# Kernel optimization log

Hardware: AMD Instinct MI355X
Metric: run time of the kernel (lower is better)

The kernel has to match this reference:

```python
import jax, jax.numpy as jnp
import numpy as np

B = 8
H_IN, W_IN = 448, 448
STRIDE = 32
NUM_CLASSES = 20
CONF_THRESH = 0.01
NMS_THRESH = 0.5
HS, WS = H_IN // STRIDE, W_IN // STRIDE  # 14, 14
N_CELLS = HS * WS  # 196
CHANNELS = [3, 64, 128, 256, 512, 512]
HEAD_OUT = 1 + NUM_CLASSES + 4  # 25


def _conv(x, w, stride):
    return jax.lax.conv_general_dilated(
        x, w, (stride, stride), 'SAME',
        dimension_numbers=('NCHW', 'OIHW', 'NCHW'))


def _create_grid():
    gy, gx = jnp.meshgrid(jnp.arange(HS), jnp.arange(WS), indexing='ij')
    return jnp.stack([gx, gy], -1).reshape(1, N_CELLS, 2).astype(jnp.float32)


def _iou_matrix(boxes):
    # boxes: [N,4] xyxy -> [N,N] pairwise IoU
    x1, y1, x2, y2 = boxes[:, 0], boxes[:, 1], boxes[:, 2], boxes[:, 3]
    area = jnp.maximum(x2 - x1, 0.0) * jnp.maximum(y2 - y1, 0.0)
    ix1 = jnp.maximum(x1[:, None], x1[None, :])
    iy1 = jnp.maximum(y1[:, None], y1[None, :])
    ix2 = jnp.minimum(x2[:, None], x2[None, :])
    iy2 = jnp.minimum(y2[:, None], y2[None, :])
    inter = jnp.maximum(ix2 - ix1, 0.0) * jnp.maximum(iy2 - iy1, 0.0)
    return inter / (area[:, None] + area[None, :] - inter + 1e-14)


def _nms_keep(scores, iou):
    # greedy per-class NMS; scores [N], iou [N,N] -> bool keep mask [N]
    order = jnp.argsort(-scores)
    iou_s = iou[order][:, order]
    idx = jnp.arange(N_CELLS)
    valid = scores[order] > CONF_THRESH

    def body(i, keep):
        sup = (iou_s[i] > NMS_THRESH) & (idx > i) & keep[i]
        return keep & (~sup)

    keep = jax.lax.fori_loop(0, N_CELLS, body, valid)
    return jnp.zeros(N_CELLS, bool).at[order].set(keep)


def setup_inputs() -> dict:
    key = jax.random.key(0)
    ks = jax.random.split(key, 8)
    x = jax.random.normal(ks[0], (B, 3, H_IN, W_IN), dtype=jnp.float32)
    params = {}
    for i in range(5):
        cin, cout = CHANNELS[i], CHANNELS[i + 1]
        std = np.sqrt(2.0 / (cin * 9))
        params[f'w{i+1}'] = jax.random.normal(ks[i + 1], (cout, cin, 3, 3), dtype=jnp.float32) * std
    std = np.sqrt(2.0 / CHANNELS[-1])
    params['w_head'] = jax.random.normal(ks[6], (HEAD_OUT, CHANNELS[-1], 1, 1), dtype=jnp.float32) * std
    return {'x': x, **params}


def reference(x, w1, w2, w3, w4, w5, w_head):
    # backbone: 5 stride-2 conv+relu stages -> stride 32
    h = x
    for w in (w1, w2, w3, w4, w5):
        h = jax.nn.relu(_conv(h, w, 2))
    pred = _conv(h, w_head, 1)                      # [B, 25, 14, 14]
    pred = pred.reshape(B, HEAD_OUT, N_CELLS).transpose(0, 2, 1)  # [B, N, 25]

    conf = jax.nn.sigmoid(pred[..., 0:1])                              # [B,N,1]
    cls_scores = jax.nn.softmax(pred[..., 1:1 + NUM_CLASSES], -1) * conf  # [B,N,C]
    txtytwth = pred[..., 1 + NUM_CLASSES:]                             # [B,N,4]

    grid = _create_grid()                                              # [1,N,2]
    xy = (jax.nn.sigmoid(txtytwth[..., :2]) + grid) * STRIDE
    wh = jnp.exp(txtytwth[..., 2:]) * STRIDE
    scale = jnp.array([W_IN, H_IN, W_IN, H_IN], dtype=jnp.float32)
    boxes = jnp.concatenate([xy - wh * 0.5, xy + wh * 0.5], -1) / scale
    boxes = jnp.clip(boxes, 0.0, 1.0)                                  # [B,N,4]

    iou = jax.vmap(_iou_matrix)(boxes)                                 # [B,N,N]
    # per-class NMS, vmapped over classes then batch
    nms_c = jax.vmap(_nms_keep, in_axes=(-1, None), out_axes=-1)       # [N,C]
    keep = jax.vmap(nms_c, in_axes=(0, 0))(cls_scores, iou)            # [B,N,C]
    final_scores = cls_scores * keep
    return jnp.concatenate([boxes, final_scores], -1)                  # [B,N,4+C]
```

## Files before the change

### kernel.cpp

```cpp
#include <hip/hip_runtime.h>
#include <math.h>

#define BATCH 8
#define NCELLS 196
#define NCLS 20
#define HEADC 25

typedef __attribute__((ext_vector_type(8))) short short8;
typedef __attribute__((ext_vector_type(4))) float f32x4;
#define MFMA16(a,b,c) __builtin_amdgcn_mfma_f32_16x16x32_bf16(a,b,c,0,0,0)

__device__ __forceinline__ unsigned short f2bf(float x) {
    union { float f; unsigned u; } a; a.f = x;
    unsigned r = a.u + 0x7FFFu + ((a.u >> 16) & 1u);
    return (unsigned short)(r >> 16);
}
__device__ __forceinline__ float bf2f(unsigned short h) {
    union { unsigned u; float f; } a; a.u = ((unsigned)h) << 16;
    return a.f;
}
__device__ __forceinline__ void split_bf(float x, unsigned short& h, unsigned short& l) {
    h = f2bf(x);
    l = f2bf(x - bf2f(h));
}

__device__ __forceinline__ void prep_one(const float* __restrict__ w, int CIN, int COUT,
                                         int idx, unsigned short* __restrict__ whi,
                                         unsigned short* __restrict__ wlo) {
    int G = COUT >> 4, CH = CIN >> 5;
    int j    = idx & 7;
    int lane = (idx >> 3) & 63;
    int fg   = idx >> 9;
    int g    = fg % G;
    int fc   = fg / G;
    int chunk = fc % CH;
    int plane = fc / CH;
    int co = g * 16 + (lane & 15);
    int ci = chunk * 32 + (lane >> 4) * 8 + j;
    int ky = plane / 3, kx = plane % 3;
    float v = w[((co * CIN + ci) * 3 + ky) * 3 + kx];
    unsigned short h, l; split_bf(v, h, l);
    whi[idx] = h; wlo[idx] = l;
}
__global__ void prep_all(const float* __restrict__ w2, const float* __restrict__ w3,
                         const float* __restrict__ w4, const float* __restrict__ w5,
                         unsigned short* __restrict__ w2h, unsigned short* __restrict__ w2l,
                         unsigned short* __restrict__ w3h, unsigned short* __restrict__ w3l,
                         unsigned short* __restrict__ w4h, unsigned short* __restrict__ w4l,
                         unsigned short* __restrict__ w5h, unsigned short* __restrict__ w5l) {
    int idx = blockIdx.x * 256 + threadIdx.x;
    const int n2 = 73728, n3 = 294912, n4 = 1179648, n5 = 2359296;
    if (idx < n2) { prep_one(w2, 64, 128, idx, w2h, w2l); return; }
    idx -= n2;
    if (idx < n3) { prep_one(w3, 128, 256, idx, w3h, w3l); return; }
    idx -= n3;
    if (idx < n4) { prep_one(w4, 256, 512, idx, w4h, w4l); return; }
    idx -= n4;
    if (idx < n5) { prep_one(w5, 512, 512, idx, w5h, w5l); }
}

__global__ void conv1_kernel(const float* __restrict__ x, const float* __restrict__ w1,
                             unsigned short* __restrict__ ohi, unsigned short* __restrict__ olo) {
    __shared__ float sW[27][64];
    __shared__ float sX[3][3][66];
    int bid = blockIdx.x;
    int xseg = bid % 7;  bid /= 7;
    int oy   = bid % 224;
    int b    = bid / 224;
    int ox0  = xseg * 32;

    for (int e = threadIdx.x; e < 1728; e += 256) {
        int k = e >> 6, co = e & 63;
        sW[k][co] = w1[co * 27 + k];
    }
    for (int e = threadIdx.x; e < 594; e += 256) {
        int ci = e / 198;
        int r  = e - ci * 198;
        int ky = r / 66;
        int lx = r - ky * 66;
        int iy = 2 * oy + ky;
        int ix = 2 * ox0 + lx;
        float v = 0.f;
        if (lx < 65 && iy < 448 && ix < 448)
            v = x[(((size_t)b * 3 + ci) * 448 + iy) * 448 + ix];
        sX[ci][ky][lx] = v;
    }
    __syncthreads();

    int pxl = threadIdx.x >> 3;
    int cog = threadIdx.x & 7;
    float acc[8] = {0.f,0.f,0.f,0.f,0.f,0.f,0.f,0.f};
    #pragma unroll
    for (int ci = 0; ci < 3; ci++) {
        #pragma unroll
        for (int ky = 0; ky < 3; ky++) {
            const float* row = sX[ci][ky];
            #pragma unroll
            for (int kx = 0; kx < 3; kx++) {
                float iv = row[2 * pxl + kx];
                int k = (ci * 3 + ky) * 3 + kx;
                float4 wa = *(const float4*)&sW[k][cog * 8];
                float4 wb = *(const float4*)&sW[k][cog * 8 + 4];
                acc[0] += wa.x * iv; acc[1] += wa.y * iv; acc[2] += wa.z * iv; acc[3] += wa.w * iv;
                acc[4] += wb.x * iv; acc[5] += wb.y * iv; acc[6] += wb.z * iv; acc[7] += wb.w * iv;
            }
        }
    }
    union { unsigned short u[8]; uint4 v; } ph, pl;
    #pragma unroll
    for (int u = 0; u < 8; u++) {
        float v = fmaxf(acc[u], 0.f);
        split_bf(v, ph.u[u], pl.u[u]);
    }
    size_t base = ((size_t)(b * 224 + oy) * 224 + ox0 + pxl) * 64 + cog * 8;
    *(uint4*)&ohi[base] = ph.v;
    *(uint4*)&olo[base] = pl.v;
}

template<int CIN, int COUT, int HIN, int WIN, int KSPLIT, bool PARTIAL>
__launch_bounds__(256, 4)
__global__ void conv_mfma(const unsigned short* __restrict__ ahi, const unsigned short* __restrict__ alo,
                          const unsigned short* __restrict__ whi, const unsigned short* __restrict__ wlo,
                          unsigned short* __restrict__ ohi, unsigned short* __restrict__ olo,
                          float* __restrict__ part) {
    constexpr int HOUT = HIN / 2, WOUT = WIN / 2;
    constexpr int TX = (WOUT + 7) / 8, TY = (HOUT + 7) / 8;
    constexpr int COG = COUT / 128;
    constexpr int CH_TOT = CIN / 32;
    constexpr int CH = CH_TOT / KSPLIT;
    constexpr int G = COUT / 16;
    constexpr int PLANE_E = 17 * 17 * 32;
    constexpr size_t PSZ = (size_t)BATCH * HOUT * WOUT * COUT;

    __shared__ __align__(16) unsigned short sA[2 * PLANE_E];

    int bid = blockIdx.x;
    int ks  = bid % KSPLIT; bid /= KSPLIT;
    int txi = bid % TX;     bid /= TX;
    int tyi = bid % TY;     bid /= TY;
    int cg  = bid % COG;
    int b   = bid / COG;
    int oy0 = tyi * 8, ox0 = txi * 8;
    int iy0 = oy0 * 2, ix0 = ox0 * 2;

    int tid = threadIdx.x;
    int w   = tid >> 6;
    int lane = tid & 63;
    int n = lane & 15, quad = lane >> 4;

    int oyl[4], oxl[4], pbase[4];
    #pragma unroll
    for (int nt = 0; nt < 4; nt++) {
        int oyq = nt >> 1, oxq = nt & 1;
        int oy_off = oyq * 4 + (n >> 2);
        int ox_off = oxq * 4 + (n & 3);
        oyl[nt] = oy0 + oy_off;
        oxl[nt] = ox0 + ox_off;
        pbase[nt] = 2 * oy_off * 17 + 2 * ox_off;
    }

    f32x4 zero = {0.f, 0.f, 0.f, 0.f};
    f32x4 acc[2][4];
    #pragma unroll
    for (int ct = 0; ct < 2; ct++)
        #pragma unroll
        for (int nt = 0; nt < 4; nt++) acc[ct][nt] = zero;

    int g0 = cg * 8 + w * 2;

    for (int ch = 0; ch < CH; ch++) {
        int chunk = ks * CH + ch;
        int ci0 = chunk * 32;
        __syncthreads();
        for (int e = tid; e < 17 * 17 * 8; e += 256) {
            int pxi = e >> 3, grp = e & 7;
            int liy = pxi / 17, lix = pxi - liy * 17;
            int iy = iy0 + liy, ix = ix0 + lix;
            uint4 v = make_uint4(0u, 0u, 0u, 0u);
            if (iy < HIN && ix < WIN) {
                const unsigned short* src = ((grp & 4) ? alo : ahi)
                    + ((size_t)(b * HIN + iy) * WIN + ix) * CIN + ci0 + (grp & 3) * 8;
                v = *(const uint4*)src;
            }
            int u = pxi * 4 + ((grp & 3) ^ ((pxi >> 1) & 3));
            *(uint4*)&sA[((grp >> 2) ? PLANE_E : 0) + u * 8] = v;
        }
        __syncthreads();
        short8 Ah[3][2], Al[3][2];
        auto loadA = [&](int pl, int slot) {
            size_t fbase = ((size_t)(pl * CH_TOT + chunk) * G + g0) * 512 + lane * 8;
            Ah[slot][0] = *(const short8*)(whi + fbase);
            Ah[slot][1] = *(const short8*)(whi + fbase + 512);
            Al[slot][0] = *(const short8*)(wlo + fbase);
            Al[slot][1] = *(const short8*)(wlo + fbase + 512);
        };
        loadA(0, 0); loadA(1, 1); loadA(2, 2);
        #pragma unroll
        for (int pl = 0; pl < 9; pl++) {
            const int slot = pl % 3;
            int dp = (pl / 3) * 17 + (pl % 3);
            #pragma unroll
            for (int nt = 0; nt < 4; nt++) {
                int p = pbase[nt] + dp;
                int u = p * 4 + (quad ^ ((p >> 1) & 3));
                short8 Bh = *(const short8*)&sA[u * 8];
                short8 Bl = *(const short8*)&sA[PLANE_E + u * 8];
                acc[0][nt] = MFMA16(Ah[slot][0], Bh, acc[0][nt]);
                acc[0][nt] = MFMA16(Ah[slot][0], Bl, acc[0][nt]);
                acc[0][nt] = MFMA16(Al[slot][0], Bh, acc[0][nt]);
                acc[1][nt] = MFMA16(Ah[slot][1], Bh, acc[1][nt]);
                acc[1][nt] = MFMA16(Ah[slot][1], Bl, acc[1][nt]);
                acc[1][nt] = MFMA16(Al[slot][1], Bh, acc[1][nt]);
            }
            if (pl + 3 < 9) loadA(pl + 3, slot);
        }
    }
    int cob = cg * 128 + w * 32;
    #pragma unroll
    for (int ct = 0; ct < 2; ct++) {
        #pragma unroll
        for (int nt = 0; nt < 4; nt++) {
            if (oyl[nt] >= HOUT || oxl[nt] >= WOUT) continue;
            size_t base = ((size_t)(b * HOUT + oyl[nt]) * WOUT + oxl[nt]) * COUT
                          + cob + ct * 16 + quad * 4;
            if (PARTIAL) {
                *(f32x4*)&part[(size_t)ks * PSZ + base] = acc[ct][nt];
            } else {
                unsigned long long h64 = 0ull, l64 = 0ull;
                #pragma unroll
                for (int r = 0; r < 4; r++) {
                    float v = fmaxf(acc[ct][nt][r], 0.f);
                    unsigned short hh, ll; split_bf(v, hh, ll);
                    h64 |= ((unsigned long long)hh) << (16 * r);
                    l64 |= ((unsigned long long)ll) << (16 * r);
                }
                *(unsigned long long*)&ohi[base] = h64;
                *(unsigned long long*)&olo[base] = l64;
            }
        }
    }
}

template<int KS>
__global__ void reduceN_split(const float* __restrict__ p, unsigned short* __restrict__ oh,
                              unsigned short* __restrict__ ol, int n) {
    int n4 = n >> 2;
    int i = blockIdx.x * 256 + threadIdx.x;
    if (i >= n4) return;
    const float4* p4 = (const float4*)p;
    float4 s = p4[i];
    #pragma unroll
    for (int k = 1; k < KS; k++) {
        float4 t = p4[i + (size_t)k * n4];
        s.x += t.x; s.y += t.y; s.z += t.z; s.w += t.w;
    }
    float v[4] = { fmaxf(s.x,0.f), fmaxf(s.y,0.f), fmaxf(s.z,0.f), fmaxf(s.w,0.f) };
    unsigned long long h64 = 0ull, l64 = 0ull;
    #pragma unroll
    for (int r = 0; r < 4; r++) {
        unsigned short hh, ll; split_bf(v[r], hh, ll);
        h64 |= ((unsigned long long)hh) << (16 * r);
        l64 |= ((unsigned long long)ll) << (16 * r);
    }
    *(unsigned long long*)&oh[i * 4] = h64;
    *(unsigned long long*)&ol[i * 4] = l64;
}

__global__ void head_decode_kernel(const unsigned short* __restrict__ ah,
                                   const unsigned short* __restrict__ al,
                                   const float* __restrict__ wh,
                                   float* __restrict__ out, float* __restrict__ cls) {
    int wave = threadIdx.x >> 6;
    int lane = threadIdx.x & 63;
    int cellid = blockIdx.x * 4 + wave;
    float acc[HEADC];
    #pragma unroll
    for (int c = 0; c < HEADC; c++) acc[c] = 0.f;
    for (int it = 0; it < 8; it++) {
        int ci = it * 64 + lane;
        size_t idx = (size_t)cellid * 512 + ci;
        float a = bf2f(ah[idx]) + bf2f(al[idx]);
        #pragma unroll
        for (int c = 0; c < HEADC; c++) acc[c] += a * wh[c * 512 + ci];
    }
    #pragma unroll
    for (int c = 0; c < HEADC; c++) {
        float v = acc[c];
        v += __shfl_down(v, 32); v += __shfl_down(v, 16); v += __shfl_down(v, 8);
        v += __shfl_down(v, 4);  v += __shfl_down(v, 2);  v += __shfl_down(v, 1);
        acc[c] = v;
    }
    if (lane == 0) {
        int cell = cellid % NCELLS;
        int gx = cell % 14, gy = cell / 14;
        float conf = 1.f / (1.f + expf(-acc[0]));
        float m = acc[1];
        #pragma unroll
        for (int c = 1; c < NCLS; c++) m = fmaxf(m, acc[1 + c]);
        float e[NCLS], s = 0.f;
        #pragma unroll
        for (int c = 0; c < NCLS; c++) { e[c] = expf(acc[1 + c] - m); s += e[c]; }
        float inv = conf / s;
        #pragma unroll
        for (int c = 0; c < NCLS; c++) cls[(size_t)cellid * NCLS + c] = e[c] * inv;
        float cx = (1.f / (1.f + expf(-acc[21])) + gx) * 32.f;
        float cy = (1.f / (1.f + expf(-acc[22])) + gy) * 32.f;
        float bw = expf(acc[23]) * 32.f;
        float bh = expf(acc[24]) * 32.f;
        float x1 = (cx - 0.5f * bw) / 448.f, y1 = (cy - 0.5f * bh) / 448.f;
        float x2 = (cx + 0.5f * bw) / 448.f, y2 = (cy + 0.5f * bh) / 448.f;
        x1 = fminf(fmaxf(x1, 0.f), 1.f); y1 = fminf(fmaxf(y1, 0.f), 1.f);
        x2 = fminf(fmaxf(x2, 0.f), 1.f); y2 = fminf(fmaxf(y2, 0.f), 1.f);
        float* o = out + (size_t)cellid * 24;
        o[0] = x1; o[1] = y1; o[2] = x2; o[3] = y2;
    }
}

__global__ void nms_kernel(const float* __restrict__ cls, const float* __restrict__ boxes,
                           float* __restrict__ out) {
    int b = blockIdx.x / NCLS;
    int c = blockIdx.x % NCLS;
    __shared__ float sc[NCELLS];
    __shared__ float ssort[NCELLS];
    __shared__ int   ord[NCELLS];
    __shared__ __align__(16) float sbox[NCELLS][4];
    __shared__ float sarea[NCELLS];
    __shared__ __align__(16) unsigned long long smask[NCELLS][4];
    int j = threadIdx.x;
    int lane = j & 63;
    int w = j >> 6;
    float sj = 0.f;
    if (j < NCELLS) {
        sj = cls[(((size_t)b * NCELLS) + j) * NCLS + c];
        sc[j] = sj;
        float4 bx = *(const float4*)&boxes[(((size_t)b * NCELLS) + j) * 24];
        *(float4*)sbox[j] = bx;
        sarea[j] = fmaxf(bx.z - bx.x, 0.f) * fmaxf(bx.w - bx.y, 0.f);
    }
    __syncthreads();
    if (j < NCELLS) {
        int r = 0;
        for (int k = 0; k < NCELLS; k++) {
            float sk = sc[k];
            r += (sk > sj) || (sk == sj && k < j);
        }
        ord[r] = j; ssort[r] = sj;
    }
    __syncthreads();
    int oc[4]; float bx1[4], by1[4], bx2[4], by2[4], bar[4];
    #pragma unroll
    for (int k = 0; k < 4; k++) {
        int cidx = k * 64 + lane;
        oc[k] = (cidx < NCELLS) ? ord[cidx] : 0;
        bx1[k] = sbox[oc[k]][0]; by1[k] = sbox[oc[k]][1];
        bx2[k] = sbox[oc[k]][2]; by2[k] = sbox[oc[k]][3];
        bar[k] = sarea[oc[k]];
    }
    for (int i = w; i < NCELLS; i += 4) {
        int oi = ord[i];
        float ix1 = sbox[oi][0], iy1 = sbox[oi][1];
        float ix2 = sbox[oi][2], iy2 = sbox[oi][3];
        float ia  = sarea[oi];
        #pragma unroll
        for (int k = 0; k < 4; k++) {
            int cidx = k * 64 + lane;
            bool sup = false;
            if (cidx < NCELLS && cidx > i) {
                float xx1 = fmaxf(ix1, bx1[k]), yy1 = fmaxf(iy1, by1[k]);
                float xx2 = fminf(ix2, bx2[k]), yy2 = fminf(iy2, by2[k]);
                float inter = fmaxf(xx2 - xx1, 0.f) * fmaxf(yy2 - yy1, 0.f);
                float iou = inter / (ia + bar[k] - inter + 1e-14f);
                sup = iou > 0.5f;
            }
            unsigned long long m = __ballot(sup);
            if (lane == 0) smask[i][k] = m;
        }
    }
    __syncthreads();
    unsigned long long keep[4];
    #pragma unroll
    for (int k = 0; k < 4; k++) {
        int cidx = k * 64 + lane;
        bool valid = (cidx < NCELLS) && (ssort[cidx] > 0.01f);
        keep[k] = __ballot(valid);
    }
    #pragma unroll
    for (int wi = 0; wi < 4; wi++) {
        int base = wi * 64;
        int lim = (NCELLS - base < 64) ? (NCELLS - base) : 64;
        for (int t = 0; t < lim; t++) {
            if ((keep[wi] >> t) & 1ull) {
                int i = base + t;
                keep[0] &= ~smask[i][0];
                keep[1] &= ~smask[i][1];
                keep[2] &= ~smask[i][2];
                keep[3] &= ~smask[i][3];
            }
        }
    }
    if (j < NCELLS) {
        bool kept = (keep[w] >> lane) & 1ull;
        out[(((size_t)b * NCELLS) + ord[j]) * 24 + 4 + c] = kept ? ssort[j] : 0.f;
    }
}

extern "C" void kernel_launch(void* const* d_in, const int* in_sizes, int n_in,
                              void* d_out, int out_size, void* d_ws, size_t ws_size,
                              hipStream_t stream) {
    const float* x  = (const float*)d_in[0];
    const float* w1 = (const float*)d_in[1];
    const float* w2 = (const float*)d_in[2];
    const float* w3 = (const float*)d_in[3];
    const float* w4 = (const float*)d_in[4];
    const float* w5 = (const float*)d_in[5];
    const float* wh = (const float*)d_in[6];
    float* out = (float*)d_out;
    char* base = (char*)d_ws;

    unsigned short* a1h = (unsigned short*)(base);
    unsigned short* a1l = a1h + 25690112;
    unsigned short* a3h = (unsigned short*)(base);
    unsigned short* a3l = a3h + 6422528;
    float* part4 = (float*)(base + 25690112);
    float* part5 = (float*)(base);
    unsigned short* a5h = (unsigned short*)(base + 51380224);
    unsigned short* a5l = a5h + 802816;
    float* clsb = (float*)(base + 54746240);
    unsigned short* a2h = (unsigned short*)(base + 102760448);
    unsigned short* a2l = a2h + 12845056;
    unsigned short* a4h = (unsigned short*)(base + 102760448);
    unsigned short* a4l = a4h + 3211264;
    unsigned short* w2h = (unsigned short*)(base + 154140672);
    unsigned short* w3h = w2h + 73728;
    unsigned short* w4h = w3h + 294912;
    unsigned short* w5h = w4h + 1179648;
    unsigned short* w2l = (unsigned short*)(base + 161955840);
    unsigned short* w3l = w2l + 73728;
    unsigned short* w4l = w3l + 294912;
    unsigned short* w5l = w4l + 1179648;

    prep_all<<<15264, 256, 0, stream>>>(w2, w3, w4, w5,
                                        w2h, w2l, w3h, w3l, w4h, w4l, w5h, w5l);

    conv1_kernel<<<12544, 256, 0, stream>>>(x, w1, a1h, a1l);

    conv_mfma<64, 128, 224, 224, 1, false><<<1568, 256, 0, stream>>>(
        a1h, a1l, w2h, w2l, a2h, a2l, nullptr);
    conv_mfma<128, 256, 112, 112, 1, false><<<784, 256, 0, stream>>>(
        a2h, a2l, w3h, w3l, a3h, a3l, nullptr);
    conv_mfma<256, 512, 56, 56, 2, true><<<1024, 256, 0, stream>>>(
        a3h, a3l, w4h, w4l, nullptr, nullptr, part4);
    reduceN_split<2><<<3136, 256, 0, stream>>>(part4, a4h, a4l, 3211264);
    conv_mfma<512, 512, 28, 28, 8, true><<<1024, 256, 0, stream>>>(
        a4h, a4l, w5h, w5l, nullptr, nullptr, part5);
    reduceN_split<8><<<784, 256, 0, stream>>>(part5, a5h, a5l, 802816);

    head_decode_kernel<<<392, 256, 0, stream>>>(a5h, a5l, wh, out, clsb);
    nms_kernel<<<160, 256, 0, stream>>>(clsb, out, out);
}
```

Measured before the change: 445.9 us.

## Fuse conv1 into conv2 MFMA kernel, recomputing conv1 tiles in shared memory

Replaces the separate conv1 kernel and the first conv_mfma launch with a fused kernel. Each block loads a 35x35x3 input patch, computes the 17x17x64 conv1 halo tile directly into the swizzled shared-memory layout in hi/lo bf16, and then runs the conv2 MFMA loop. This removes the large a1 intermediate write and read (about 100MB of bf16 hi/lo traffic), at the cost of recomputing halo pixels and doing scalar FP32 conv1 work inside the MFMA kernel. Separately, the generic conv_mfma drops its three-slot weight-register prefetch ring and loads weights inside each plane iteration, which may expose load latency.

```diff
diff --git a/kernel.cpp b/kernel.cpp
--- a/kernel.cpp
+++ b/kernel.cpp
@@ -59,62 +59,139 @@
     if (idx < n5) { prep_one(w5, 512, 512, idx, w5h, w5l); }
 }
 
-__global__ void conv1_kernel(const float* __restrict__ x, const float* __restrict__ w1,
-                             unsigned short* __restrict__ ohi, unsigned short* __restrict__ olo) {
-    __shared__ float sW[27][64];
-    __shared__ float sX[3][3][66];
+__launch_bounds__(256, 2)
+__global__ void conv2_fused(const float* __restrict__ x, const float* __restrict__ w1,
+                            const unsigned short* __restrict__ whi, const unsigned short* __restrict__ wlo,
+                            unsigned short* __restrict__ ohi, unsigned short* __restrict__ olo) {
+    constexpr int PLANE_E = 17 * 17 * 32;
+    __shared__ __align__(16) unsigned short sA[2 * PLANE_E];
+    __shared__ float sX[3][35][36];
+    __shared__ float sW1[27][64];
+
     int bid = blockIdx.x;
-    int xseg = bid % 7;  bid /= 7;
-    int oy   = bid % 224;
-    int b    = bid / 224;
-    int ox0  = xseg * 32;
-
-    for (int e = threadIdx.x; e < 1728; e += 256) {
-        int k = e >> 6, co = e & 63;
-        sW[k][co] = w1[co * 27 + k];
-    }
-    for (int e = threadIdx.x; e < 594; e += 256) {
-        int ci = e / 198;
-        int r  = e - ci * 198;
-        int ky = r / 66;
-        int lx = r - ky * 66;
-        int iy = 2 * oy + ky;
-        int ix = 2 * ox0 + lx;
+    int txi = bid % 14;  bid /= 14;
+    int tyi = bid % 14;
+    int b   = bid / 14;
+    int oy0 = tyi * 8, ox0 = txi * 8;
+    int ay0 = oy0 * 2, ax0 = ox0 * 2;
+    int xy0 = ay0 * 2, xx0 = ax0 * 2;
+
+    int tid = threadIdx.x;
+    int w   = tid >> 6;
+    int lane = tid & 63;
+    int n = lane & 15, quad = lane >> 4;
+
+    for (int e = tid; e < 1728; e += 256)
+        sW1[e >> 6][e & 63] = w1[(e & 63) * 27 + (e >> 6)];
+    for (int e = tid; e < 3675; e += 256) {
+        int ci = e / 1225;
+        int r  = (e / 35) % 35;
+        int cx = e % 35;
         float v = 0.f;
-        if (lx < 65 && iy < 448 && ix < 448)
-            v = x[(((size_t)b * 3 + ci) * 448 + iy) * 448 + ix];
-        sX[ci][ky][lx] = v;
-    }
-    __syncthreads();
-
-    int pxl = threadIdx.x >> 3;
-    int cog = threadIdx.x & 7;
-    float acc[8] = {0.f,0.f,0.f,0.f,0.f,0.f,0.f,0.f};
-    #pragma unroll
-    for (int ci = 0; ci < 3; ci++) {
-        #pragma unroll
-        for (int ky = 0; ky < 3; ky++) {
-            const float* row = sX[ci][ky];
+        if (xy0 + r < 448 && xx0 + cx < 448)
+            v = x[(((size_t)b * 3 + ci) * 448 + xy0 + r) * 448 + xx0 + cx];
+        sX[ci][r][cx] = v;
+    }
+
+    int oyl[4], oxl[4], pbase[4];
+    #pragma unroll
+    for (int nt = 0; nt < 4; nt++) {
+        int oy_off = (nt >> 1) * 4 + (n >> 2);
+        int ox_off = (nt & 1) * 4 + (n & 3);
+        oyl[nt] = oy0 + oy_off;
+        oxl[nt] = ox0 + ox_off;
+        pbase[nt] = 2 * oy_off * 17 + 2 * ox_off;
+    }
+    f32x4 zero = {0.f, 0.f, 0.f, 0.f};
+    f32x4 acc[2][4];
+    #pragma unroll
+    for (int ct = 0; ct < 2; ct++)
+        #pragma unroll
+        for (int nt = 0; nt < 4; nt++) acc[ct][nt] = zero;
+    int g0 = w * 2;
+
+    for (int ch = 0; ch < 2; ch++) {
+        __syncthreads();
+        for (int e = tid; e < 289 * 4; e += 256) {
+            int pxi = e >> 2, g = e & 3;
+            int liy = pxi / 17, lix = pxi - liy * 17;
+            int co8 = ch * 32 + g * 8;
+            union { unsigned short u[8]; uint4 v; } ph, pl;
+            if (ay0 + liy < 224 && ax0 + lix < 224) {
+                float a0[8] = {0.f,0.f,0.f,0.f,0.f,0.f,0.f,0.f};
+                #pragma unroll
+                for (int ci = 0; ci < 3; ci++)
+                    #pragma unroll
+                    for (int ky = 0; ky < 3; ky++) {
+                        const float* row = sX[ci][2 * liy + ky];
+                        #pragma unroll
+                        for (int kx = 0; kx < 3; kx++) {
+                            float xv = row[2 * lix + kx];
+                            const float* wp = &sW1[ci * 9 + ky * 3 + kx][co8];
+                            float4 wa = *(const float4*)wp;
+                            float4 wb = *(const float4*)(wp + 4);
+                            a0[0] += wa.x * xv; a0[1] += wa.y * xv;
+                            a0[2] += wa.z * xv; a0[3] += wa.w * xv;
+                            a0[4] += wb.x * xv; a0[5] += wb.y * xv;
+                            a0[6] += wb.z * xv; a0[7] += wb.w * xv;
+                        }
+                    }
+                #pragma unroll
+                for (int u = 0; u < 8; u++) {
+                    float v = fmaxf(a0[u], 0.f);
+                    split_bf(v, ph.u[u], pl.u[u]);
+                }
+            } else {
+                ph.v = make_uint4(0u,0u,0u,0u);
+                pl.v = make_uint4(0u,0u,0u,0u);
+            }
+            int u = pxi * 4 + (g ^ ((pxi >> 1) & 3));
+            *(uint4*)&sA[u * 8] = ph.v;
+            *(uint4*)&sA[PLANE_E + u * 8] = pl.v;
+        }
+        __syncthreads();
+        #pragma unroll
+        for (int pl = 0; pl < 9; pl++) {
+            size_t fbase = ((size_t)(pl * 2 + ch) * 8 + g0) * 512 + lane * 8;
+            short8 Ah0 = *(const short8*)(whi + fbase);
+            short8 Ah1 = *(const short8*)(whi + fbase + 512);
+            short8 Al0 = *(const short8*)(wlo + fbase);
+            short8 Al1 = *(const short8*)(wlo + fbase + 512);
+            int dp = (pl / 3) * 17 + (pl % 3);
             #pragma unroll
-            for (int kx = 0; kx < 3; kx++) {
-                float iv = row[2 * pxl + kx];
-                int k = (ci * 3 + ky) * 3 + kx;
-                float4 wa = *(const float4*)&sW[k][cog * 8];
-                float4 wb = *(const float4*)&sW[k][cog * 8 + 4];
-                acc[0] += wa.x * iv; acc[1] += wa.y * iv; acc[2] += wa.z * iv; acc[3] += wa.w * iv;
-                acc[4] += wb.x * iv; acc[5] += wb.y * iv; acc[6] += wb.z * iv; acc[7] += wb.w * iv;
-            }
-        }
-    }
-    union { unsigned short u[8]; uint4 v; } ph, pl;
-    #pragma unroll
-    for (int u = 0; u < 8; u++) {
-        float v = fmaxf(acc[u], 0.f);
-        split_bf(v, ph.u[u], pl.u[u]);
-    }
-    size_t base = ((size_t)(b * 224 + oy) * 224 + ox0 + pxl) * 64 + cog * 8;
-    *(uint4*)&ohi[base] = ph.v;
-    *(uint4*)&olo[base] = pl.v;
+            for (int nt = 0; nt < 4; nt++) {
+                int p = pbase[nt] + dp;
+                int u = p * 4 + (quad ^ ((p >> 1) & 3));
+                short8 Bh = *(const short8*)&sA[u * 8];
+                short8 Bl = *(const short8*)&sA[PLANE_E + u * 8];
+                acc[0][nt] = MFMA16(Ah0, Bh, acc[0][nt]);
+                acc[0][nt] = MFMA16(Ah0, Bl, acc[0][nt]);
+                acc[0][nt] = MFMA16(Al0, Bh, acc[0][nt]);
+                acc[1][nt] = MFMA16(Ah1, Bh, acc[1][nt]);
+                acc[1][nt] = MFMA16(Ah1, Bl, acc[1][nt]);
+                acc[1][nt] = MFMA16(Al1, Bh, acc[1][nt]);
+            }
+        }
+    }
+    int cob = w * 32;
+    #pragma unroll
+    for (int ct = 0; ct < 2; ct++) {
+        #pragma unroll
+        for (int nt = 0; nt < 4; nt++) {
+            size_t base = ((size_t)(b * 112 + oyl[nt]) * 112 + oxl[nt]) * 128
+                          + cob + ct * 16 + quad * 4;
+            unsigned long long h64 = 0ull, l64 = 0ull;
+            #pragma unroll
+            for (int r = 0; r < 4; r++) {
+                float v = fmaxf(acc[ct][nt][r], 0.f);
+                unsigned short hh, ll; split_bf(v, hh, ll);
+                h64 |= ((unsigned long long)hh) << (16 * r);
+                l64 |= ((unsigned long long)ll) << (16 * r);
+            }
+            *(unsigned long long*)&ohi[base] = h64;
+            *(unsigned long long*)&olo[base] = l64;
+        }
+    }
 }
 
 template<int CIN, int COUT, int HIN, int WIN, int KSPLIT, bool PARTIAL>
@@ -186,18 +263,13 @@
             *(uint4*)&sA[((grp >> 2) ? PLANE_E : 0) + u * 8] = v;
         }
         __syncthreads();
-        short8 Ah[3][2], Al[3][2];
-        auto loadA = [&](int pl, int slot) {
+        #pragma unroll
+        for (int pl = 0; pl < 9; pl++) {
             size_t fbase = ((size_t)(pl * CH_TOT + chunk) * G + g0) * 512 + lane * 8;
-            Ah[slot][0] = *(const short8*)(whi + fbase);
-            Ah[slot][1] = *(const short8*)(whi + fbase + 512);
-            Al[slot][0] = *(const short8*)(wlo + fbase);
-            Al[slot][1] = *(const short8*)(wlo + fbase + 512);
-        };
-        loadA(0, 0); loadA(1, 1); loadA(2, 2);
-        #pragma unroll
-        for (int pl = 0; pl < 9; pl++) {
-            const int slot = pl % 3;
+            short8 Ah0 = *(const short8*)(whi + fbase);
+            short8 Ah1 = *(const short8*)(whi + fbase + 512);
+            short8 Al0 = *(const short8*)(wlo + fbase);
+            short8 Al1 = *(const short8*)(wlo + fbase + 512);
             int dp = (pl / 3) * 17 + (pl % 3);
             #pragma unroll
             for (int nt = 0; nt < 4; nt++) {
@@ -205,14 +277,13 @@
                 int u = p * 4 + (quad ^ ((p >> 1) & 3));
                 short8 Bh = *(const short8*)&sA[u * 8];
                 short8 Bl = *(const short8*)&sA[PLANE_E + u * 8];
-                acc[0][nt] = MFMA16(Ah[slot][0], Bh, acc[0][nt]);
-                acc[0][nt] = MFMA16(Ah[slot][0], Bl, acc[0][nt]);
-                acc[0][nt] = MFMA16(Al[slot][0], Bh, acc[0][nt]);
-                acc[1][nt] = MFMA16(Ah[slot][1], Bh, acc[1][nt]);
-                acc[1][nt] = MFMA16(Ah[slot][1], Bl, acc[1][nt]);
-                acc[1][nt] = MFMA16(Al[slot][1], Bh, acc[1][nt]);
-            }
-            if (pl + 3 < 9) loadA(pl + 3, slot);
+                acc[0][nt] = MFMA16(Ah0, Bh, acc[0][nt]);
+                acc[0][nt] = MFMA16(Ah0, Bl, acc[0][nt]);
+                acc[0][nt] = MFMA16(Al0, Bh, acc[0][nt]);
+                acc[1][nt] = MFMA16(Ah1, Bh, acc[1][nt]);
+                acc[1][nt] = MFMA16(Ah1, Bl, acc[1][nt]);
+                acc[1][nt] = MFMA16(Al1, Bh, acc[1][nt]);
+            }
         }
     }
     int cob = cg * 128 + w * 32;
@@ -417,8 +488,6 @@
     float* out = (float*)d_out;
     char* base = (char*)d_ws;
 
-    unsigned short* a1h = (unsigned short*)(base);
-    unsigned short* a1l = a1h + 25690112;
     unsigned short* a3h = (unsigned short*)(base);
     unsigned short* a3l = a3h + 6422528;
     float* part4 = (float*)(base + 25690112);
@@ -442,10 +511,8 @@
     prep_all<<<15264, 256, 0, stream>>>(w2, w3, w4, w5,
                                         w2h, w2l, w3h, w3l, w4h, w4l, w5h, w5l);
 
-    conv1_kernel<<<12544, 256, 0, stream>>>(x, w1, a1h, a1l);
-
-    conv_mfma<64, 128, 224, 224, 1, false><<<1568, 256, 0, stream>>>(
-        a1h, a1l, w2h, w2l, a2h, a2l, nullptr);
+    conv2_fused<<<1568, 256, 0, stream>>>(x, w1, w2h, w2l, a2h, a2l);
+
     conv_mfma<128, 256, 112, 112, 1, false><<<784, 256, 0, stream>>>(
         a2h, a2l, w3h, w3l, a3h, a3l, nullptr);
     conv_mfma<256, 512, 56, 56, 2, true><<<1024, 256, 0, stream>>>(
```

Result: faster. 436.5 us (-2.1%).
